# Performance work log

Measured on AMD Instinct MI355X. Metric: run time of the kernel, lower is better.

The kernel has to match this reference:

```python
import jax, jax.numpy as jnp
import numpy as np

N_EMBED = 1024
D_TOTAL = 512      # n_output_embed
N_GRID = 16        # n_output_size
H = 8              # n_heads
D_HEAD = D_TOTAL // H
HIDDEN = 4 * D_TOTAL
INIT_STD = 0.02


def setup_inputs() -> dict:
    key = jax.random.key(0)
    ks = jax.random.split(key, 12)
    s = INIT_STD
    return {
        "x": jax.random.normal(ks[0], (8, 4096, N_EMBED), dtype=jnp.float32),
        "mask": jnp.ones((8, 4096), dtype=bool),
        "W_kv": s * jax.random.normal(ks[1], (N_EMBED, 2 * D_TOTAL), dtype=jnp.float32),
        "b_kv": s * jax.random.normal(ks[2], (2 * D_TOTAL,), dtype=jnp.float32),
        "row_query": s * jax.random.normal(ks[3], (N_GRID, D_TOTAL // 2), dtype=jnp.float32),
        "col_query": s * jax.random.normal(ks[4], (N_GRID, D_TOTAL // 2), dtype=jnp.float32),
        "query_projection": s * jax.random.normal(ks[5], (D_TOTAL, D_TOTAL), dtype=jnp.float32),
        "W1": s * jax.random.normal(ks[6], (D_TOTAL, HIDDEN), dtype=jnp.float32),
        "b1": s * jax.random.normal(ks[7], (HIDDEN,), dtype=jnp.float32),
        "W2": s * jax.random.normal(ks[8], (HIDDEN, D_TOTAL), dtype=jnp.float32),
        "b2": s * jax.random.normal(ks[9], (D_TOTAL,), dtype=jnp.float32),
    }


def reference(x, mask, W_kv, b_kv, row_query, col_query, query_projection, W1, b1, W2, b2):
    b, s_len, _ = x.shape
    N, dt = N_GRID, D_TOTAL
    # Faithful to torch.einsum('ij,bnj->bnj', W, x): contract W over axis 0 only,
    # i.e. elementwise scale of x by W.sum(0). (Requires n_embed == 2*n_output_embed.)
    kv = x * jnp.sum(W_kv, axis=0) + b_kv                 # (b, s, 2*dt)
    k = kv[..., :dt].reshape(b, s_len, H, D_HEAD)
    v = kv[..., dt:].reshape(b, s_len, H, D_HEAD)
    # Grid queries: concat row/col halves, project.
    qg = jnp.concatenate([
        jnp.broadcast_to(row_query[:, None, :], (N, N, dt // 2)),
        jnp.broadcast_to(col_query[None, :, :], (N, N, dt // 2)),
    ], axis=2).reshape(N * N, dt)
    qg = (qg @ query_projection).reshape(N * N, H, D_HEAD)  # (q, h, d)
    # Scores over the sequence (no 1/sqrt(d) scaling in the original).
    scores = jnp.einsum('bshd,qhd->bshq', k, qg)           # (b, s, h, N*N)
    scores = jnp.where(mask[:, :, None, None], scores, -jnp.inf)
    att = jax.nn.softmax(scores, axis=1)                   # softmax over seq dim
    agg = jnp.einsum('bshd,bshq->bqhd', v, att).reshape(b, N * N, dt)
    # Residual MLP (dropout = 0, eval mode).
    mlp = jax.nn.gelu(agg @ W1 + b1) @ W2 + b2
    out = (agg + mlp).reshape(b, N, N, dt)
    return out
```

## Files before the change

kernel.cpp:

```cpp
#include <hip/hip_runtime.h>
#include <hip/hip_bf16.h>

typedef float f32x4 __attribute__((ext_vector_type(4)));
typedef __bf16 bf16x8 __attribute__((ext_vector_type(8)));
typedef unsigned short u16;
typedef u16 u16x8 __attribute__((ext_vector_type(8)));
typedef u16 u16x4 __attribute__((ext_vector_type(4)));
typedef unsigned int u32;
typedef u32 u32x4 __attribute__((ext_vector_type(4)));

__device__ __forceinline__ u16 f2bf(float f) {
  unsigned int u = __builtin_bit_cast(unsigned int, f);
  u += 0x7fffu + ((u >> 16) & 1u);
  return (u16)(u >> 16);
}
__device__ __forceinline__ float bf2f(u16 v) {
  return __builtin_bit_cast(float, (unsigned int)v << 16);
}
__device__ __forceinline__ unsigned int pack2(float a, float b) {
  return (unsigned int)f2bf(a) | ((unsigned int)f2bf(b) << 16);
}
__device__ __forceinline__ f32x4 mfma_bf16(u16x8 a, u16x8 b, f32x4 c) {
  return __builtin_amdgcn_mfma_f32_16x16x32_bf16(
      __builtin_bit_cast(bf16x8, a), __builtin_bit_cast(bf16x8, b), c, 0, 0, 0);
}
__device__ __forceinline__ void gload16(const u16* g, u16* l) {
  __builtin_amdgcn_global_load_lds((const __attribute__((address_space(1))) void*)g,
                                   (__attribute__((address_space(3))) void*)l, 16, 0, 0);
}

__global__ void colsum1_kernel(const float* __restrict__ Wkv, float* __restrict__ wpart) {
  int bl = blockIdx.x, tid = threadIdx.x;
  float a[4] = {0.f, 0.f, 0.f, 0.f};
  for (int r = 0; r < 8; ++r) {
    int base = (bl * 8 + r) * 1024;
#pragma unroll
    for (int cc = 0; cc < 4; ++cc) a[cc] += Wkv[base + cc * 256 + tid];
  }
#pragma unroll
  for (int cc = 0; cc < 4; ++cc) wpart[bl * 1024 + cc * 256 + tid] = a[cc];
}
__global__ void colsum2_kernel(const float* __restrict__ wpart, float* __restrict__ wsum) {
  int c = blockIdx.x * 256 + threadIdx.x;
  float s = 0.f;
  for (int bl = 0; bl < 128; ++bl) s += wpart[bl * 1024 + c];
  wsum[c] = s;
}

__global__ void rowcol_part_kernel(const float* __restrict__ rq, const float* __restrict__ cq,
                                   const float* __restrict__ P, float* __restrict__ rpart) {
  int blk = blockIdx.x;
  int half = blk >> 7, i = (blk >> 3) & 15, cseg = blk & 7;
  int tid = threadIdx.x;
  const float* qsrc = half ? cq : rq;
  float a0 = 0.f, a1 = 0.f;
  for (int cc = 0; cc < 32; ++cc) {
    int c = cseg * 32 + cc;
    float val = qsrc[i * 256 + c];
    int crow = half ? (256 + c) : c;
    a0 += val * P[crow * 512 + tid];
    a1 += val * P[crow * 512 + tid + 256];
  }
  int hi = half * 16 + i;
  rpart[(cseg * 32 + hi) * 512 + tid] = a0;
  rpart[(cseg * 32 + hi) * 512 + tid + 256] = a1;
}
__global__ void rowred_kernel(const float* __restrict__ rpart, float* __restrict__ AB) {
  int idx = blockIdx.x * 256 + threadIdx.x;
  int hi = idx >> 9, col = idx & 511;
  float s = 0.f;
#pragma unroll
  for (int cseg = 0; cseg < 8; ++cseg) s += rpart[(cseg * 32 + hi) * 512 + col];
  AB[hi * 512 + col] = s;
}

__global__ __launch_bounds__(256) void transp_kernel(const float* __restrict__ src,
                                                     u16* __restrict__ dst, int R, int C) {
  __shared__ float t[64][65];
  int c0 = blockIdx.x * 64, r0 = blockIdx.y * 64;
  int tid = threadIdx.x;
  int col = tid & 63, rw = tid >> 6;
#pragma unroll
  for (int j = 0; j < 16; ++j) {
    int row = j * 4 + rw;
    t[row][col] = src[(size_t)(r0 + row) * C + c0 + col];
  }
  __syncthreads();
#pragma unroll
  for (int j = 0; j < 16; ++j) {
    int row = j * 4 + rw;
    dst[(size_t)(c0 + row) * R + r0 + col] = f2bf(t[col][row]);
  }
}

__global__ __launch_bounds__(512, 4) void attn_partial_kernel(
    const float* __restrict__ x, const float* __restrict__ wsum,
    const float* __restrict__ bkv, const float* __restrict__ AB,
    u16* __restrict__ part_o, float* __restrict__ part_d) {
  const int j = blockIdx.x;
  const int q = j >> 6;
  const int r = j & 63;
  const int grp = q * 8 + (r & 7);
  const int h = r >> 3;
  const int b = grp >> 3;
  const int ch = grp & 7;
  const int tid = threadIdx.x;
  const int w = tid >> 6;
  const int l = tid & 63;
  const int l16 = l & 15;
  const int g = l >> 4;
  const int hl = l >> 5;
  const int li = l & 31;
  const int d2 = li << 1;

  __shared__ u16 Klds[2][64 * 72];
  __shared__ u16 Vt[2][64 * 72];

  const int hb = h * 64;
  const float2 wk = *(const float2*)&wsum[hb + d2];
  const float2 bk2 = *(const float2*)&bkv[hb + d2];
  const float wvl = wsum[512 + hb + l];
  const float bvl = bkv[512 + hb + l];

  u16x8 qf[2][2];
#pragma unroll
  for (int nt = 0; nt < 2; ++nt) {
#pragma unroll
    for (int kk = 0; kk < 2; ++kk) {
      int qq = w * 32 + nt * 16 + l16;
      int col = hb + kk * 32 + g * 8;
      float4 ra = *(const float4*)&AB[(qq >> 4) * 512 + col];
      float4 rb = *(const float4*)&AB[(qq >> 4) * 512 + col + 4];
      float4 ca = *(const float4*)&AB[(16 + (qq & 15)) * 512 + col];
      float4 cb = *(const float4*)&AB[(16 + (qq & 15)) * 512 + col + 4];
      u16x8 f;
      f[0] = f2bf(ra.x + ca.x); f[1] = f2bf(ra.y + ca.y);
      f[2] = f2bf(ra.z + ca.z); f[3] = f2bf(ra.w + ca.w);
      f[4] = f2bf(rb.x + cb.x); f[5] = f2bf(rb.y + cb.y);
      f[6] = f2bf(rb.z + cb.z); f[7] = f2bf(rb.w + cb.w);
      qf[nt][kk] = f;
    }
  }

  f32x4 acc[4][2];
#pragma unroll
  for (int da = 0; da < 4; ++da)
#pragma unroll
    for (int nt = 0; nt < 2; ++nt) acc[da][nt] = (f32x4){0.f, 0.f, 0.f, 0.f};
  float dsum[2] = {0.f, 0.f};

  const int sbase = b * 4096 + ch * 512;

  float2 kreg[4];
  float vreg[8];

  auto LOAD = [&](int t) {
    const int s0 = sbase + t * 64;
#pragma unroll
    for (int jj = 0; jj < 4; ++jj) {
      int row = w * 8 + jj * 2 + hl;
      kreg[jj] = *(const float2*)&x[(size_t)(s0 + row) * 1024 + hb + d2];
    }
#pragma unroll
    for (int jp = 0; jp < 4; ++jp) {
      int rr = w * 8 + jp * 2;
      vreg[2 * jp]     = x[(size_t)(s0 + rr) * 1024 + 512 + hb + l];
      vreg[2 * jp + 1] = x[(size_t)(s0 + rr + 1) * 1024 + 512 + hb + l];
    }
  };
  auto STORE = [&](int buf) {
#pragma unroll
    for (int jj = 0; jj < 4; ++jj) {
      int row = w * 8 + jj * 2 + hl;
      int rowp = (row & 35) | ((row & 4) << 2) | ((row & 24) >> 1);
      *(unsigned int*)&Klds[buf][rowp * 72 + d2] =
          pack2(fmaf(kreg[jj].x, wk.x, bk2.x), fmaf(kreg[jj].y, wk.y, bk2.y));
    }
#pragma unroll
    for (int jp = 0; jp < 4; ++jp) {
      int rr = w * 8 + jp * 2;
      *(unsigned int*)&Vt[buf][l * 72 + rr] =
          pack2(fmaf(vreg[2 * jp], wvl, bvl), fmaf(vreg[2 * jp + 1], wvl, bvl));
    }
  };

  LOAD(0);
  STORE(0);
  __syncthreads();
  int cur = 0;

  for (int t = 0; t < 8; ++t) {
    if (t < 7) LOAD(t + 1);

    u32x4 pbv[2][2];
#pragma unroll
    for (int mss = 0; mss < 4; ++mss) {
      const int kk = mss >> 1, mu = mss & 1;
      u16x8 ka0 = *(const u16x8*)&Klds[cur][(mss * 16 + l16) * 72 + g * 8];
      u16x8 ka1 = *(const u16x8*)&Klds[cur][(mss * 16 + l16) * 72 + 32 + g * 8];
#pragma unroll
      for (int nt = 0; nt < 2; ++nt) {
        f32x4 s = (f32x4){0.f, 0.f, 0.f, 0.f};
        s = mfma_bf16(ka0, qf[nt][0], s);
        s = mfma_bf16(ka1, qf[nt][1], s);
        float p0 = __expf(s[0]);
        float p1 = __expf(s[1]);
        float p2 = __expf(s[2]);
        float p3 = __expf(s[3]);
        dsum[nt] += (p0 + p1) + (p2 + p3);
        pbv[nt][kk][2 * mu]     = pack2(p0, p1);
        pbv[nt][kk][2 * mu + 1] = pack2(p2, p3);
      }
    }

#pragma unroll
    for (int da = 0; da < 4; ++da) {
      u16x8 va0 = *(const u16x8*)&Vt[cur][(da * 16 + l16) * 72 + g * 8];
      u16x8 va1 = *(const u16x8*)&Vt[cur][(da * 16 + l16) * 72 + 32 + g * 8];
#pragma unroll
      for (int nt = 0; nt < 2; ++nt) {
        acc[da][nt] = mfma_bf16(va0, __builtin_bit_cast(u16x8, pbv[nt][0]), acc[da][nt]);
        acc[da][nt] = mfma_bf16(va1, __builtin_bit_cast(u16x8, pbv[nt][1]), acc[da][nt]);
      }
    }

    if (t < 7) {
      STORE(cur ^ 1);
      __syncthreads();
      cur ^= 1;
    }
  }

  const int bhch = (b * 8 + h) * 8 + ch;
#pragma unroll
  for (int nt = 0; nt < 2; ++nt) {
    float dv = dsum[nt];
    dv += __shfl_xor(dv, 16);
    dv += __shfl_xor(dv, 32);
    if (l < 16) part_d[bhch * 256 + w * 32 + nt * 16 + l] = dv;
  }
#pragma unroll
  for (int da = 0; da < 4; ++da)
#pragma unroll
    for (int nt = 0; nt < 2; ++nt) {
      int qq = w * 32 + nt * 16 + l16;
      int dd = da * 16 + g * 4;
      u16x4 o4;
      o4[0] = f2bf(acc[da][nt][0]);
      o4[1] = f2bf(acc[da][nt][1]);
      o4[2] = f2bf(acc[da][nt][2]);
      o4[3] = f2bf(acc[da][nt][3]);
      *(u16x4*)&part_o[((size_t)bhch * 256 + qq) * 64 + dd] = o4;
    }
}

__global__ void combine_kernel(const u16* __restrict__ part_o,
                               const float* __restrict__ part_d,
                               float* __restrict__ agg, u16* __restrict__ aggb) {
  int idx = blockIdx.x * 256 + threadIdx.x;
  int c = idx & 511;
  int q = (idx >> 9) & 255;
  int b = idx >> 17;
  int h = c >> 6, d = c & 63;
  int bh = b * 8 + h;
  float o = 0.f, den = 0.f;
#pragma unroll
  for (int ch = 0; ch < 8; ++ch) {
    o += bf2f(part_o[((size_t)(bh * 8 + ch) * 256 + q) * 64 + d]);
    den += part_d[(bh * 8 + ch) * 256 + q];
  }
  float r = o / den;
  agg[idx] = r;
  aggb[idx] = f2bf(r);
}

__device__ __forceinline__ void gemm_main(const u16* __restrict__ A, const u16* __restrict__ B,
                                          int K, int m0, int n0, int k0, int nit,
                                          u16* Alds, u16* Blds, f32x4 (&acc)[4][2],
                                          int w, int l) {
  const int wm = w >> 1, wn = w & 1;
  const int l16 = l & 15, g = l >> 4;
  const int lr = l >> 3, lc = (l & 7) * 8;
  for (int it = 0; it < nit; ++it) {
    int kb = k0 + it * 64;
    if (it) __syncthreads();
#pragma unroll
    for (int i = 0; i < 4; ++i) {
      int r = i * 32 + w * 8 + lr;
      gload16(&A[(size_t)(m0 + r) * K + kb + lc], &Alds[(i * 32 + w * 8) * 64]);
    }
#pragma unroll
    for (int i = 0; i < 2; ++i) {
      int r = i * 32 + w * 8 + lr;
      gload16(&B[(size_t)(n0 + r) * K + kb + lc], &Blds[(i * 32 + w * 8) * 64]);
    }
    __syncthreads();
#pragma unroll
    for (int kk = 0; kk < 2; ++kk) {
      u16x8 af[4], bf[2];
#pragma unroll
      for (int mi = 0; mi < 4; ++mi)
        af[mi] = *(const u16x8*)&Alds[(wm * 64 + mi * 16 + l16) * 64 + kk * 32 + g * 8];
#pragma unroll
      for (int ni = 0; ni < 2; ++ni)
        bf[ni] = *(const u16x8*)&Blds[(wn * 32 + ni * 16 + l16) * 64 + kk * 32 + g * 8];
#pragma unroll
      for (int mi = 0; mi < 4; ++mi)
#pragma unroll
        for (int ni = 0; ni < 2; ++ni)
          acc[mi][ni] = mfma_bf16(af[mi], bf[ni], acc[mi][ni]);
    }
  }
}

__global__ __launch_bounds__(256) void gemm1_kernel(
    const u16* __restrict__ aggb, const u16* __restrict__ W1t,
    const float* __restrict__ b1, u16* __restrict__ h1) {
  __shared__ u16 Alds[128 * 64];
  __shared__ u16 Blds[64 * 64];
  const int m0 = blockIdx.x * 128, n0 = blockIdx.y * 64;
  const int tid = threadIdx.x, w = tid >> 6, l = tid & 63;
  f32x4 acc[4][2];
#pragma unroll
  for (int mi = 0; mi < 4; ++mi)
#pragma unroll
    for (int ni = 0; ni < 2; ++ni) acc[mi][ni] = (f32x4){0.f, 0.f, 0.f, 0.f};
  gemm_main(aggb, W1t, 512, m0, n0, 0, 8, Alds, Blds, acc, w, l);
  const int wm = w >> 1, wn = w & 1, l16 = l & 15, g = l >> 4;
#pragma unroll
  for (int ni = 0; ni < 2; ++ni) {
    int n = n0 + wn * 32 + ni * 16 + l16;
    float bias = b1[n];
#pragma unroll
    for (int mi = 0; mi < 4; ++mi)
#pragma unroll
      for (int r = 0; r < 4; ++r) {
        int m = m0 + wm * 64 + mi * 16 + g * 4 + r;
        float u = acc[mi][ni][r] + bias;
        float z = 0.7978845608028654f * (u + 0.044715f * u * u * u);
        float e = __expf(2.f * z);
        float t = 1.f - 2.f * __builtin_amdgcn_rcpf(e + 1.f);
        h1[(size_t)m * 2048 + n] = f2bf(0.5f * u * (1.f + t));
      }
  }
}

__global__ __launch_bounds__(256) void gemm2_kernel(
    const u16* __restrict__ h1, const u16* __restrict__ W2t,
    float* __restrict__ part2) {
  __shared__ u16 Alds[128 * 64];
  __shared__ u16 Blds[64 * 64];
  const int m0 = blockIdx.x * 128, n0 = blockIdx.y * 64;
  const int split = blockIdx.z;
  const int tid = threadIdx.x, w = tid >> 6, l = tid & 63;
  f32x4 acc[4][2];
#pragma unroll
  for (int mi = 0; mi < 4; ++mi)
#pragma unroll
    for (int ni = 0; ni < 2; ++ni) acc[mi][ni] = (f32x4){0.f, 0.f, 0.f, 0.f};
  gemm_main(h1, W2t, 2048, m0, n0, split * 512, 8, Alds, Blds, acc, w, l);
  const int wm = w >> 1, wn = w & 1, l16 = l & 15, g = l >> 4;
  float* pbase = part2 + (size_t)split * 2048 * 512;
#pragma unroll
  for (int ni = 0; ni < 2; ++ni) {
    int n = n0 + wn * 32 + ni * 16 + l16;
#pragma unroll
    for (int mi = 0; mi < 4; ++mi)
#pragma unroll
      for (int r = 0; r < 4; ++r) {
        int m = m0 + wm * 64 + mi * 16 + g * 4 + r;
        pbase[(size_t)m * 512 + n] = acc[mi][ni][r];
      }
  }
}

__global__ void combine2_kernel(const float* __restrict__ part2, const float* __restrict__ b2,
                                const float* __restrict__ agg, float* __restrict__ out) {
  int idx = blockIdx.x * 256 + threadIdx.x;
  int e = idx * 4;
  int n = e & 511;
  float4 s = *(const float4*)&part2[e];
  float4 s1 = *(const float4*)&part2[1048576 + e];
  float4 s2 = *(const float4*)&part2[2097152 + e];
  float4 s3 = *(const float4*)&part2[3145728 + e];
  float4 bb = *(const float4*)&b2[n];
  float4 aa = *(const float4*)&agg[e];
  float4 o;
  o.x = s.x + s1.x + s2.x + s3.x + bb.x + aa.x;
  o.y = s.y + s1.y + s2.y + s3.y + bb.y + aa.y;
  o.z = s.z + s1.z + s2.z + s3.z + bb.z + aa.z;
  o.w = s.w + s1.w + s2.w + s3.w + bb.w + aa.w;
  *(float4*)&out[e] = o;
}

extern "C" void kernel_launch(void* const* d_in, const int* in_sizes, int n_in,
                              void* d_out, int out_size, void* d_ws, size_t ws_size,
                              hipStream_t stream) {
  const float* x   = (const float*)d_in[0];
  const float* Wkv = (const float*)d_in[2];
  const float* bkv = (const float*)d_in[3];
  const float* rq  = (const float*)d_in[4];
  const float* cq  = (const float*)d_in[5];
  const float* qp  = (const float*)d_in[6];
  const float* W1  = (const float*)d_in[7];
  const float* b1  = (const float*)d_in[8];
  const float* W2  = (const float*)d_in[9];
  const float* b2  = (const float*)d_in[10];
  float* out = (float*)d_out;

  float* ws = (float*)d_ws;
  float* wsum   = ws;
  float* wpart  = ws + 4096;
  float* rpart  = ws + 139264;
  float* AB     = ws + 274432;
  float* agg    = ws + 294912;
  u16*   part_o = (u16*)(ws + 1347584);
  float* part2  = ws + 1347584;
  float* part_d = ws + 5545984;
  u16*   h1     = (u16*)(ws + 5681152);
  u16*   W1t    = (u16*)(ws + 7782400);
  u16*   W2t    = (u16*)(ws + 8310784);
  u16*   aggb   = (u16*)(ws + 8839168);

  colsum1_kernel<<<128, 256, 0, stream>>>(Wkv, wpart);
  colsum2_kernel<<<4, 256, 0, stream>>>(wpart, wsum);
  rowcol_part_kernel<<<256, 256, 0, stream>>>(rq, cq, qp, rpart);
  rowred_kernel<<<64, 256, 0, stream>>>(rpart, AB);
  transp_kernel<<<dim3(32, 8), 256, 0, stream>>>(W1, W1t, 512, 2048);
  transp_kernel<<<dim3(8, 32), 256, 0, stream>>>(W2, W2t, 2048, 512);
  attn_partial_kernel<<<512, 512, 0, stream>>>(x, wsum, bkv, AB, part_o, part_d);
  combine_kernel<<<4096, 256, 0, stream>>>(part_o, part_d, agg, aggb);
  gemm1_kernel<<<dim3(16, 32), 256, 0, stream>>>(aggb, W1t, b1, h1);
  gemm2_kernel<<<dim3(16, 8, 4), 256, 0, stream>>>(h1, W2t, part2);
  combine2_kernel<<<1024, 256, 0, stream>>>(part2, b2, agg, out);
}
```

Measured before the change: 95.33 us.

## Fold K/V affine scaling into queries and combine step, use exp2

Moves the per-channel key scale into the bf16 query fragments and turns the key bias into a per-query constant added before the exponent. The value scale and bias are applied after normalisation in the combine kernel, which is exact because softmax weights sum to one. The staging loop now only packs raw x into LDS, with no FMAs. The log2(e) factor is folded into the queries so the kernel can call exp2f. The block index mapping is also simplified. Risk: bf16 rounding now happens on raw x rather than on the scaled values, which changes numerics slightly.

After: 104.5 us. +9.7%, slower.

```diff
diff --git a/kernel.cpp b/kernel.cpp
--- a/kernel.cpp
+++ b/kernel.cpp
@@ -1,5 +1,6 @@
 #include <hip/hip_runtime.h>
 #include <hip/hip_bf16.h>
+#include <math.h>
 
 typedef float f32x4 __attribute__((ext_vector_type(4)));
 typedef __bf16 bf16x8 __attribute__((ext_vector_type(8)));
@@ -97,13 +98,10 @@
     const float* __restrict__ x, const float* __restrict__ wsum,
     const float* __restrict__ bkv, const float* __restrict__ AB,
     u16* __restrict__ part_o, float* __restrict__ part_d) {
-  const int j = blockIdx.x;
-  const int q = j >> 6;
-  const int r = j & 63;
-  const int grp = q * 8 + (r & 7);
-  const int h = r >> 3;
-  const int b = grp >> 3;
-  const int ch = grp & 7;
+  const int blk = blockIdx.x;
+  const int b = blk >> 6;
+  const int h = (blk >> 3) & 7;
+  const int ch = blk & 7;
   const int tid = threadIdx.x;
   const int w = tid >> 6;
   const int l = tid & 63;
@@ -117,29 +115,41 @@
   __shared__ u16 Vt[2][64 * 72];
 
   const int hb = h * 64;
-  const float2 wk = *(const float2*)&wsum[hb + d2];
-  const float2 bk2 = *(const float2*)&bkv[hb + d2];
-  const float wvl = wsum[512 + hb + l];
-  const float bvl = bkv[512 + hb + l];
+  const float LOG2E = 1.4426950408889634f;
 
   u16x8 qf[2][2];
+  float cq[2] = {0.f, 0.f};
 #pragma unroll
   for (int nt = 0; nt < 2; ++nt) {
 #pragma unroll
-    for (int kk = 0; kk < 2; ++kk) {
+    for (int kq = 0; kq < 2; ++kq) {
       int qq = w * 32 + nt * 16 + l16;
-      int col = hb + kk * 32 + g * 8;
+      int col = hb + kq * 32 + g * 8;
       float4 ra = *(const float4*)&AB[(qq >> 4) * 512 + col];
       float4 rb = *(const float4*)&AB[(qq >> 4) * 512 + col + 4];
       float4 ca = *(const float4*)&AB[(16 + (qq & 15)) * 512 + col];
       float4 cb = *(const float4*)&AB[(16 + (qq & 15)) * 512 + col + 4];
+      float4 wa = *(const float4*)&wsum[col];
+      float4 wb = *(const float4*)&wsum[col + 4];
+      float4 ba = *(const float4*)&bkv[col];
+      float4 bb = *(const float4*)&bkv[col + 4];
+      float q0 = ra.x + ca.x, q1 = ra.y + ca.y, q2 = ra.z + ca.z, q3 = ra.w + ca.w;
+      float q4 = rb.x + cb.x, q5 = rb.y + cb.y, q6 = rb.z + cb.z, q7 = rb.w + cb.w;
       u16x8 f;
-      f[0] = f2bf(ra.x + ca.x); f[1] = f2bf(ra.y + ca.y);
-      f[2] = f2bf(ra.z + ca.z); f[3] = f2bf(ra.w + ca.w);
-      f[4] = f2bf(rb.x + cb.x); f[5] = f2bf(rb.y + cb.y);
-      f[6] = f2bf(rb.z + cb.z); f[7] = f2bf(rb.w + cb.w);
-      qf[nt][kk] = f;
-    }
+      f[0] = f2bf(q0 * wa.x * LOG2E); f[1] = f2bf(q1 * wa.y * LOG2E);
+      f[2] = f2bf(q2 * wa.z * LOG2E); f[3] = f2bf(q3 * wa.w * LOG2E);
+      f[4] = f2bf(q4 * wb.x * LOG2E); f[5] = f2bf(q5 * wb.y * LOG2E);
+      f[6] = f2bf(q6 * wb.z * LOG2E); f[7] = f2bf(q7 * wb.w * LOG2E);
+      qf[nt][kq] = f;
+      cq[nt] += q0 * ba.x + q1 * ba.y + q2 * ba.z + q3 * ba.w +
+                q4 * bb.x + q5 * bb.y + q6 * bb.z + q7 * bb.w;
+    }
+  }
+#pragma unroll
+  for (int nt = 0; nt < 2; ++nt) {
+    cq[nt] += __shfl_xor(cq[nt], 16);
+    cq[nt] += __shfl_xor(cq[nt], 32);
+    cq[nt] *= LOG2E;
   }
 
   f32x4 acc[4][2];
@@ -173,14 +183,12 @@
     for (int jj = 0; jj < 4; ++jj) {
       int row = w * 8 + jj * 2 + hl;
       int rowp = (row & 35) | ((row & 4) << 2) | ((row & 24) >> 1);
-      *(unsigned int*)&Klds[buf][rowp * 72 + d2] =
-          pack2(fmaf(kreg[jj].x, wk.x, bk2.x), fmaf(kreg[jj].y, wk.y, bk2.y));
+      *(unsigned int*)&Klds[buf][rowp * 72 + d2] = pack2(kreg[jj].x, kreg[jj].y);
     }
 #pragma unroll
     for (int jp = 0; jp < 4; ++jp) {
       int rr = w * 8 + jp * 2;
-      *(unsigned int*)&Vt[buf][l * 72 + rr] =
-          pack2(fmaf(vreg[2 * jp], wvl, bvl), fmaf(vreg[2 * jp + 1], wvl, bvl));
+      *(unsigned int*)&Vt[buf][l * 72 + rr] = pack2(vreg[2 * jp], vreg[2 * jp + 1]);
     }
   };
 
@@ -203,10 +211,10 @@
         f32x4 s = (f32x4){0.f, 0.f, 0.f, 0.f};
         s = mfma_bf16(ka0, qf[nt][0], s);
         s = mfma_bf16(ka1, qf[nt][1], s);
-        float p0 = __expf(s[0]);
-        float p1 = __expf(s[1]);
-        float p2 = __expf(s[2]);
-        float p3 = __expf(s[3]);
+        float p0 = exp2f(s[0] + cq[nt]);
+        float p1 = exp2f(s[1] + cq[nt]);
+        float p2 = exp2f(s[2] + cq[nt]);
+        float p3 = exp2f(s[3] + cq[nt]);
         dsum[nt] += (p0 + p1) + (p2 + p3);
         pbv[nt][kk][2 * mu]     = pack2(p0, p1);
         pbv[nt][kk][2 * mu + 1] = pack2(p2, p3);
@@ -256,6 +264,8 @@
 
 __global__ void combine_kernel(const u16* __restrict__ part_o,
                                const float* __restrict__ part_d,
+                               const float* __restrict__ wsum,
+                               const float* __restrict__ bkv,
                                float* __restrict__ agg, u16* __restrict__ aggb) {
   int idx = blockIdx.x * 256 + threadIdx.x;
   int c = idx & 511;
@@ -269,7 +279,7 @@
     o += bf2f(part_o[((size_t)(bh * 8 + ch) * 256 + q) * 64 + d]);
     den += part_d[(bh * 8 + ch) * 256 + q];
   }
-  float r = o / den;
+  float r = wsum[512 + c] * (o / den) + bkv[512 + c];
   agg[idx] = r;
   aggb[idx] = f2bf(r);
 }
@@ -429,7 +439,7 @@
   transp_kernel<<<dim3(32, 8), 256, 0, stream>>>(W1, W1t, 512, 2048);
   transp_kernel<<<dim3(8, 32), 256, 0, stream>>>(W2, W2t, 2048, 512);
   attn_partial_kernel<<<512, 512, 0, stream>>>(x, wsum, bkv, AB, part_o, part_d);
-  combine_kernel<<<4096, 256, 0, stream>>>(part_o, part_d, agg, aggb);
+  combine_kernel<<<4096, 256, 0, stream>>>(part_o, part_d, wsum, bkv, agg, aggb);
   gemm1_kernel<<<dim3(16, 32), 256, 0, stream>>>(aggb, W1t, b1, h1);
   gemm2_kernel<<<dim3(16, 8, 4), 256, 0, stream>>>(h1, W2t, part2);
   combine2_kernel<<<1024, 256, 0, stream>>>(part2, b2, agg, out);
```
